# Kernel tuning notes

Hardware: AMD Instinct MI355X
Metric: run time of the kernel (lower is better)

Reference implementation:

```python
import jax, jax.numpy as jnp
import numpy as np

B, V, C = 8192, 512, 16  # batch, num_variables, constraints per variable
N1 = V + 1  # augmented with bias column


def setup_inputs() -> dict:
    key = jax.random.key(0)
    k1, k2, k3 = jax.random.split(key, 3)
    preds = jax.random.normal(k1, (B, V), dtype=jnp.float32)
    # Acyclic structure: variable v's constraints only reference earlier
    # variables (columns < v) plus the bias column (column V).
    cols = jnp.arange(N1)[None, :]              # [1, N1]
    vids = jnp.arange(V)[:, None]               # [V, 1]
    mask = ((cols < vids) | (cols == V)).astype(jnp.float32)[:, None, :]  # [V,1,N1]
    scale = 0.1
    pos_mats = jax.random.normal(k2, (V, C, N1), dtype=jnp.float32) * scale * mask
    neg_mats = jax.random.normal(k3, (V, C, N1), dtype=jnp.float32) * scale * mask
    return {"preds": preds, "pos_mats": pos_mats, "neg_mats": neg_mats}


def reference(preds, pos_mats, neg_mats):
    # Augment preds with a ones column (bias), as in the original __call__.
    b = preds.shape[0]
    p0 = jnp.concatenate([preds, jnp.ones((b, 1), preds.dtype)], axis=1)  # [B, N1]
    var_ids = jnp.arange(pos_mats.shape[0])

    def step(p, xs):
        pm, nm, v = xs  # pm, nm: [C, N1]
        # apply_matrix: (preds * matrix).sum(-1) with max / min reduction over C
        lower = jnp.einsum('bn,cn->bc', p, pm).max(axis=1)  # [B]
        upper = jnp.einsum('bn,cn->bc', p, nm).min(axis=1)  # [B]
        # get_final_x_correction: clamp prediction into [lower, upper]
        corrected = jnp.minimum(jnp.maximum(p[:, v], lower), upper)
        p = p.at[:, v].set(corrected)
        return p, None

    pf, _ = jax.lax.scan(step, p0, (pos_mats, neg_mats, var_ids))
    return pf[:, : preds.shape[1]]
```

## Files before the change

kernel.cpp:

```cpp
#include <hip/hip_runtime.h>

#define BATCH 8192
#define V 512
#define N1 513
#define KCH 16
#define NCHUNKS 32
#define RB 16
#define NT 1024
#define PKS 520
#define SJ2 516

typedef __bf16 bf16_t;
typedef bf16_t bf16x8 __attribute__((ext_vector_type(8)));
typedef float f32x4 __attribute__((ext_vector_type(4)));

#define EPP 4194304ull
#define DV_OFF (EPP * 2ull)
#define BV_OFF (DV_OFF + 1048576ull)

__device__ __forceinline__ f32x4 mfma16(bf16x8 a, bf16x8 b, f32x4 c) {
    return __builtin_amdgcn_mfma_f32_16x16x32_bf16(a, b, c, 0, 0, 0);
}

__device__ __forceinline__ float bcast_lane(float x, int l) {
    return __int_as_float(__builtin_amdgcn_readlane(__float_as_int(x), l));
}

__device__ __forceinline__ float dpp_xor1_max(float x) {
    const int xi = __float_as_int(x);
    const float o = __int_as_float(
        __builtin_amdgcn_update_dpp(xi, xi, 0xB1, 0xF, 0xF, false));
    return fmaxf(x, o);
}

__global__ __launch_bounds__(1024)
void repack_all(const float* __restrict__ pos, const float* __restrict__ neg,
                bf16_t* __restrict__ Mhi, float* __restrict__ Dv,
                float* __restrict__ Bv)
{
    __shared__ float sb[2 * 256 * 36];
    const int bx  = blockIdx.x;
    const int tid = threadIdx.x;
    if (bx < 496) {
        const int cc  = (bx >> 4) + 1;
        const int kb  = bx & 15;
        const int nkb = (cc + 1) >> 1;
        if (kb >= nkb) return;
        const int klen = 16 * cc;
        for (int idx = tid; idx < 8192; idx += 1024) {
            const int r = idx >> 5, k32 = idx & 31;
            const int k = kb * 32 + k32;
            const size_t row = (size_t)cc * 256 + r;
            float xp = 0.0f, xn = 0.0f;
            if (k < klen) {
                xp = pos[row * N1 + k];
                xn = -neg[row * N1 + k];
            }
            sb[r * 36 + k32]            = xp;
            sb[256 * 36 + r * 36 + k32] = xn;
        }
        __syncthreads();
        const size_t base = 16384ull * (size_t)((cc * cc) / 4) + (size_t)kb * 16384ull;
        for (int e8 = tid; e8 < 2048; e8 += 1024) {
            const int t = e8 >> 6, s = e8 & 63;
            const int c = s & 15, q = s >> 4;
            const int vloc = t >> 1, m = t & 1;
            const float* sp = &sb[m * 256 * 36 + (vloc * 16 + c) * 36 + 8 * q];
            bf16x8 o;
            #pragma unroll
            for (int jj = 0; jj < 8; ++jj) o[jj] = (bf16_t)sp[jj];
            *(bf16x8*)(Mhi + base + (size_t)e8 * 8) = o;
        }
    } else {
        const int cc = bx - 496;
        float* bufP = sb;
        float* bufN = sb + 256 * 17;
        for (int idx = tid; idx < 4096; idx += 1024) {
            const int r = idx >> 4, kk = idx & 15;
            const size_t row = (size_t)(cc * 256 + r);
            bufP[r * 17 + kk] = pos[row * N1 + cc * 16 + kk];
            bufN[r * 17 + kk] = neg[row * N1 + cc * 16 + kk];
        }
        __syncthreads();
        for (int idx = tid; idx < 8192; idx += 1024) {
            const int vl = idx >> 9, j = idx & 511;
            const int vlo = j >> 5, c = j & 15;
            const int m = (j >> 4) & 1;
            const float x = (m ? bufN : bufP)[(vlo * 16 + c) * 17 + vl];
            Dv[(size_t)cc * 8192 + idx] = m ? -x : x;
        }
        for (int j = tid; j < 512; j += 1024) {
            const int vlo = j >> 5, c = j & 15;
            const int m = (j >> 4) & 1;
            const float* src = m ? neg : pos;
            const float x = src[(size_t)(cc * 256 + vlo * 16 + c) * N1 + V];
            Bv[(size_t)cc * 512 + j] = m ? -x : x;
        }
    }
}

__global__ __launch_bounds__(NT, 8)
void shield_fused(const float* __restrict__ preds,
                  const bf16_t* __restrict__ Mhi,
                  const float* __restrict__ Dv, const float* __restrict__ Bv,
                  float* __restrict__ out)
{
    __shared__ bf16_t Phi[RB * PKS];
    __shared__ float  S[RB * SJ2];

    const int tid  = threadIdx.x;
    const int b0   = blockIdx.x * RB;
    const int lane = tid & 63;
    const int w    = tid >> 6;
    const int cq   = lane & 15;
    const int q    = lane >> 4;

    {
        const float* prow = preds + (size_t)(b0 + w) * V + lane * 8;
        const float4 p0 = *(const float4*)(prow);
        const float4 p1 = *(const float4*)(prow + 4);
        const int n = lane * 8;
        Phi[w * PKS + n + 0] = (bf16_t)p0.x;
        Phi[w * PKS + n + 1] = (bf16_t)p0.y;
        Phi[w * PKS + n + 2] = (bf16_t)p0.z;
        Phi[w * PKS + n + 3] = (bf16_t)p0.w;
        Phi[w * PKS + n + 4] = (bf16_t)p1.x;
        Phi[w * PKS + n + 5] = (bf16_t)p1.y;
        Phi[w * PKS + n + 6] = (bf16_t)p1.z;
        Phi[w * PKS + n + 7] = (bf16_t)p1.w;
    }

    int tJ[2];
    #pragma unroll
    for (int tt = 0; tt < 2; ++tt) tJ[tt] = ((2 * w + tt) << 4) + cq;
    const int aoff = cq * PKS + 8 * q;

    f32x4 acc[2];
    #pragma unroll
    for (int tt = 0; tt < 2; ++tt) {
        const float b = Bv[tJ[tt]];
        acc[tt] = f32x4{b, b, b, b};
    }

    #pragma unroll 1
    for (int cc = 0; cc < NCHUNKS; ++cc) {
        const int v0 = cc * 16;
        const int  ccn  = cc + 1;
        const bool hasN = ccn < NCHUNKS;
        const int  nkbN = hasN ? ((ccn + 1) >> 1) : 0;
        const bf16_t* phN = Mhi + 16384ull * (size_t)((ccn * ccn) / 4)
                          + (size_t)lane * 8 + (size_t)(2 * w) * 512;

        #pragma unroll
        for (int tt = 0; tt < 2; ++tt)
            #pragma unroll
            for (int reg = 0; reg < 4; ++reg)
                S[(4 * q + reg) * SJ2 + tJ[tt]] = acc[tt][reg];
        __syncthreads();

        float s2[8];
        {
            const float* sp = &S[w * SJ2 + 8 * lane];
            const float4 a0 = *(const float4*)(sp);
            const float4 a1 = *(const float4*)(sp + 4);
            s2[0] = a0.x; s2[1] = a0.y; s2[2] = a0.z; s2[3] = a0.w;
            s2[4] = a1.x; s2[5] = a1.y; s2[6] = a1.z; s2[7] = a1.w;
        }

        const bf16x8 po0 = *(const bf16x8*)(Phi + w * PKS + v0);
        const bf16x8 po1 = *(const bf16x8*)(Phi + w * PKS + v0 + 8);

        if (hasN) {
            #pragma unroll
            for (int tt = 0; tt < 2; ++tt) {
                const float b = Bv[(ccn << 9) + tJ[tt]];
                acc[tt] = f32x4{b, b, b, b};
            }
        }

        __syncthreads();

        {
            const float* src = Dv + (((size_t)cc * 16 + w) << 9) + 8 * lane;
            const float4 a = *(const float4*)(src);
            const float4 b = *(const float4*)(src + 4);
            float* dst = S + w * 512 + 8 * lane;
            *(float4*)(dst)     = a;
            *(float4*)(dst + 4) = b;
        }
        __syncthreads();

        #pragma unroll
        for (int vl = 0; vl < KCH; ++vl) {
            const int vcur = v0 + vl;
            const bool doKb = hasN && (vl < nkbN - 1);

            bf16x8 fa, fb0, fb1;
            if (doKb) {
                const int k0 = vl * 32;
                fa  = *(const bf16x8*)(Phi + aoff + k0);
                const bf16_t* pb = phN + (size_t)k0 * 512;
                fb0 = *(const bf16x8*)(pb);
                fb1 = *(const bf16x8*)(pb + 512);
            }

            float dv[8];
            {
                const float* dls = S + vl * 512 + 8 * lane;
                const float4 d0 = *(const float4*)(dls);
                const float4 d1 = *(const float4*)(dls + 4);
                dv[0]=d0.x; dv[1]=d0.y; dv[2]=d0.z; dv[3]=d0.w;
                dv[4]=d1.x; dv[5]=d1.y; dv[6]=d1.z; dv[7]=d1.w;
            }
            const float po = (float)(vl < 8 ? po0[vl & 7] : po1[vl & 7]);

            const float m0 = fmaxf(fmaxf(s2[0], s2[1]), s2[2]);
            const float m1 = fmaxf(fmaxf(s2[3], s2[4]), s2[5]);
            const float m2 = fmaxf(s2[6], s2[7]);
            const float red = dpp_xor1_max(fmaxf(fmaxf(m0, m1), m2));
            const float lw  = bcast_lane(red, 4 * vl);
            const float nup = bcast_lane(red, 4 * vl + 2);
            const float pc  = fminf(fmaxf(po, lw), -nup);
            if (lane == 4 * vl) Phi[w * PKS + vcur] = (bf16_t)pc;

            #pragma unroll
            for (int jj = 0; jj < 8; ++jj) s2[jj] = fmaf(dv[jj], pc, s2[jj]);

            if (doKb) {
                acc[0] = mfma16(fa, fb0, acc[0]);
                acc[1] = mfma16(fa, fb1, acc[1]);
            }
        }

        __syncthreads();

        if (hasN) {
            const int k0 = (nkbN - 1) * 32;
            const bf16x8 fa  = *(const bf16x8*)(Phi + aoff + k0);
            const bf16_t* pb = phN + (size_t)k0 * 512;
            const bf16x8 fb0 = *(const bf16x8*)(pb);
            const bf16x8 fb1 = *(const bf16x8*)(pb + 512);
            acc[0] = mfma16(fa, fb0, acc[0]);
            acc[1] = mfma16(fa, fb1, acc[1]);
        }
    }

    {
        float* orow = out + (size_t)(b0 + w) * V + lane * 8;
        const int n = lane * 8;
        float4 o0, o1;
        o0.x = (float)Phi[w * PKS + n + 0];
        o0.y = (float)Phi[w * PKS + n + 1];
        o0.z = (float)Phi[w * PKS + n + 2];
        o0.w = (float)Phi[w * PKS + n + 3];
        o1.x = (float)Phi[w * PKS + n + 4];
        o1.y = (float)Phi[w * PKS + n + 5];
        o1.z = (float)Phi[w * PKS + n + 6];
        o1.w = (float)Phi[w * PKS + n + 7];
        *(float4*)(orow)     = o0;
        *(float4*)(orow + 4) = o1;
    }
}

extern "C" void kernel_launch(void* const* d_in, const int* in_sizes, int n_in,
                              void* d_out, int out_size, void* d_ws, size_t ws_size,
                              hipStream_t stream) {
    const float* preds = (const float*)d_in[0];
    const float* pos   = (const float*)d_in[1];
    const float* neg   = (const float*)d_in[2];
    float* o = (float*)d_out;
    char* base = (char*)d_ws;
    bf16_t* Mhi = (bf16_t*)base;
    float*  Dv  = (float*)(base + DV_OFF);
    float*  Bv  = (float*)(base + BV_OFF);
    repack_all<<<dim3(528), 1024, 0, stream>>>(pos, neg, Mhi, Dv, Bv);
    shield_fused<<<dim3(BATCH / RB), NT, 0, stream>>>(preds, Mhi, Dv, Bv, o);
}
```

Measured before the change: 356.5 us.

## Swizzle shared-memory S layout and prefetch Dv chunk before the barrier

Applies an XOR swizzle (lane bit 2) to the float4 addresses used to write and read the S shared buffer, for both the accumulator transpose and the Dv staging. The aim is to cut LDS bank conflicts on the strided 8-float-per-lane accesses. It also issues the global Dv loads at the top of each chunk iteration, so their latency overlaps the S transpose and barriers. The cost is extra address arithmetic and two more float4 registers held live across the barriers.

```diff
diff --git a/kernel.cpp b/kernel.cpp
--- a/kernel.cpp
+++ b/kernel.cpp
@@ -114,6 +114,7 @@
     const int w    = tid >> 6;
     const int cq   = lane & 15;
     const int q    = lane >> 4;
+    const int sw4  = lane & 4;
 
     {
         const float* prow = preds + (size_t)(b0 + w) * V + lane * 8;
@@ -130,9 +131,12 @@
         Phi[w * PKS + n + 7] = (bf16_t)p1.w;
     }
 
-    int tJ[2];
+    int tJ[2], tJs[2];
     #pragma unroll
-    for (int tt = 0; tt < 2; ++tt) tJ[tt] = ((2 * w + tt) << 4) + cq;
+    for (int tt = 0; tt < 2; ++tt) {
+        tJ[tt]  = ((2 * w + tt) << 4) + cq;
+        tJs[tt] = ((2 * w + tt) << 4) + (cq ^ ((w & 1) << 2));
+    }
     const int aoff = cq * PKS + 8 * q;
 
     f32x4 acc[2];
@@ -151,18 +155,25 @@
         const bf16_t* phN = Mhi + 16384ull * (size_t)((ccn * ccn) / 4)
                           + (size_t)lane * 8 + (size_t)(2 * w) * 512;
 
+        float4 dsa, dsb;
+        {
+            const float* src = Dv + (((size_t)cc * 16 + w) << 9) + 8 * lane;
+            dsa = *(const float4*)(src);
+            dsb = *(const float4*)(src + 4);
+        }
+
         #pragma unroll
         for (int tt = 0; tt < 2; ++tt)
             #pragma unroll
             for (int reg = 0; reg < 4; ++reg)
-                S[(4 * q + reg) * SJ2 + tJ[tt]] = acc[tt][reg];
+                S[(4 * q + reg) * SJ2 + tJs[tt]] = acc[tt][reg];
         __syncthreads();
 
         float s2[8];
         {
-            const float* sp = &S[w * SJ2 + 8 * lane];
-            const float4 a0 = *(const float4*)(sp);
-            const float4 a1 = *(const float4*)(sp + 4);
+            const float* sp = &S[w * SJ2];
+            const float4 a0 = *(const float4*)(sp + ((8 * lane) ^ sw4));
+            const float4 a1 = *(const float4*)(sp + ((8 * lane + 4) ^ sw4));
             s2[0] = a0.x; s2[1] = a0.y; s2[2] = a0.z; s2[3] = a0.w;
             s2[4] = a1.x; s2[5] = a1.y; s2[6] = a1.z; s2[7] = a1.w;
         }
@@ -181,12 +192,9 @@
         __syncthreads();
 
         {
-            const float* src = Dv + (((size_t)cc * 16 + w) << 9) + 8 * lane;
-            const float4 a = *(const float4*)(src);
-            const float4 b = *(const float4*)(src + 4);
-            float* dst = S + w * 512 + 8 * lane;
-            *(float4*)(dst)     = a;
-            *(float4*)(dst + 4) = b;
+            float* dst = S + w * 512;
+            *(float4*)(dst + ((8 * lane) ^ sw4))     = dsa;
+            *(float4*)(dst + ((8 * lane + 4) ^ sw4)) = dsb;
         }
         __syncthreads();
 
@@ -206,9 +214,9 @@
 
             float dv[8];
             {
-                const float* dls = S + vl * 512 + 8 * lane;
-                const float4 d0 = *(const float4*)(dls);
-                const float4 d1 = *(const float4*)(dls + 4);
+                const float* dls = S + vl * 512;
+                const float4 d0 = *(const float4*)(dls + ((8 * lane) ^ sw4));
+                const float4 d1 = *(const float4*)(dls + ((8 * lane + 4) ^ sw4));
                 dv[0]=d0.x; dv[1]=d0.y; dv[2]=d0.z; dv[3]=d0.w;
                 dv[4]=d1.x; dv[5]=d1.y; dv[6]=d1.z; dv[7]=d1.w;
             }
```

Result: slower. 366.9 us (+2.9%).

## Process four batch rows per wave with 32-row blocks and prefetched B fragments

Applied to the files above, without the earlier changes.

Doubles the batch rows per block to 32 and halves the threads to 512 (8 waves), so each wave now runs the sequential clamp for four rows at once using f32x4 vector max/fma, and does a 2x4 MFMA tile per k-step instead of 1x2. This reuses each B fragment loaded from global memory across twice as many rows and amortises per-step scalar work. It also software-prefetches the next B fragments and the next Dv row from shared memory. It trades more registers per thread (launch bounds relaxed to 2 blocks) and a larger shared memory footprint for fewer blocks and more instruction-level parallelism, which may lower occupancy.

```diff
diff --git a/kernel.cpp b/kernel.cpp
--- a/kernel.cpp
+++ b/kernel.cpp
@@ -5,8 +5,8 @@
 #define N1 513
 #define KCH 16
 #define NCHUNKS 32
-#define RB 16
-#define NT 1024
+#define RB 32
+#define NT 512
 #define PKS 520
 #define SJ2 516
 
@@ -99,7 +99,7 @@
     }
 }
 
-__global__ __launch_bounds__(NT, 8)
+__global__ __launch_bounds__(NT, 2)
 void shield_fused(const float* __restrict__ preds,
                   const bf16_t* __restrict__ Mhi,
                   const float* __restrict__ Dv, const float* __restrict__ Bv,
@@ -114,32 +114,37 @@
     const int w    = tid >> 6;
     const int cq   = lane & 15;
     const int q    = lane >> 4;
-
-    {
-        const float* prow = preds + (size_t)(b0 + w) * V + lane * 8;
+    const int rp0  = w * 4;
+
+    #pragma unroll
+    for (int i = 0; i < 4; ++i) {
+        const int row = rp0 + i;
+        const float* prow = preds + (size_t)(b0 + row) * V + lane * 8;
         const float4 p0 = *(const float4*)(prow);
         const float4 p1 = *(const float4*)(prow + 4);
         const int n = lane * 8;
-        Phi[w * PKS + n + 0] = (bf16_t)p0.x;
-        Phi[w * PKS + n + 1] = (bf16_t)p0.y;
-        Phi[w * PKS + n + 2] = (bf16_t)p0.z;
-        Phi[w * PKS + n + 3] = (bf16_t)p0.w;
-        Phi[w * PKS + n + 4] = (bf16_t)p1.x;
-        Phi[w * PKS + n + 5] = (bf16_t)p1.y;
-        Phi[w * PKS + n + 6] = (bf16_t)p1.z;
-        Phi[w * PKS + n + 7] = (bf16_t)p1.w;
-    }
-
-    int tJ[2];
+        Phi[row * PKS + n + 0] = (bf16_t)p0.x;
+        Phi[row * PKS + n + 1] = (bf16_t)p0.y;
+        Phi[row * PKS + n + 2] = (bf16_t)p0.z;
+        Phi[row * PKS + n + 3] = (bf16_t)p0.w;
+        Phi[row * PKS + n + 4] = (bf16_t)p1.x;
+        Phi[row * PKS + n + 5] = (bf16_t)p1.y;
+        Phi[row * PKS + n + 6] = (bf16_t)p1.z;
+        Phi[row * PKS + n + 7] = (bf16_t)p1.w;
+    }
+
+    int tJ[4];
     #pragma unroll
-    for (int tt = 0; tt < 2; ++tt) tJ[tt] = ((2 * w + tt) << 4) + cq;
-    const int aoff = cq * PKS + 8 * q;
-
-    f32x4 acc[2];
+    for (int tt = 0; tt < 4; ++tt) tJ[tt] = ((4 * w + tt) << 4) + cq;
+    const int aoff0 = cq * PKS + 8 * q;
+    const int aoff1 = (16 + cq) * PKS + 8 * q;
+
+    f32x4 acc[2][4];
     #pragma unroll
-    for (int tt = 0; tt < 2; ++tt) {
+    for (int tt = 0; tt < 4; ++tt) {
         const float b = Bv[tJ[tt]];
-        acc[tt] = f32x4{b, b, b, b};
+        acc[0][tt] = f32x4{b, b, b, b};
+        acc[1][tt] = f32x4{b, b, b, b};
     }
 
     #pragma unroll 1
@@ -149,86 +154,152 @@
         const bool hasN = ccn < NCHUNKS;
         const int  nkbN = hasN ? ((ccn + 1) >> 1) : 0;
         const bf16_t* phN = Mhi + 16384ull * (size_t)((ccn * ccn) / 4)
-                          + (size_t)lane * 8 + (size_t)(2 * w) * 512;
+                          + (size_t)lane * 8 + (size_t)(4 * w) * 512;
 
         #pragma unroll
-        for (int tt = 0; tt < 2; ++tt)
-            #pragma unroll
-            for (int reg = 0; reg < 4; ++reg)
-                S[(4 * q + reg) * SJ2 + tJ[tt]] = acc[tt][reg];
-        __syncthreads();
-
-        float s2[8];
+        for (int tt = 0; tt < 4; ++tt)
+            #pragma unroll
+            for (int reg = 0; reg < 4; ++reg) {
+                S[(4 * q + reg) * SJ2 + tJ[tt]]      = acc[0][tt][reg];
+                S[(16 + 4 * q + reg) * SJ2 + tJ[tt]] = acc[1][tt][reg];
+            }
+        __syncthreads();
+
+        f32x4 s2[8];
         {
-            const float* sp = &S[w * SJ2 + 8 * lane];
+            const float* sp = &S[rp0 * SJ2 + 8 * lane];
             const float4 a0 = *(const float4*)(sp);
             const float4 a1 = *(const float4*)(sp + 4);
-            s2[0] = a0.x; s2[1] = a0.y; s2[2] = a0.z; s2[3] = a0.w;
-            s2[4] = a1.x; s2[5] = a1.y; s2[6] = a1.z; s2[7] = a1.w;
-        }
-
-        const bf16x8 po0 = *(const bf16x8*)(Phi + w * PKS + v0);
-        const bf16x8 po1 = *(const bf16x8*)(Phi + w * PKS + v0 + 8);
+            const float4 b0_ = *(const float4*)(sp + SJ2);
+            const float4 b1_ = *(const float4*)(sp + SJ2 + 4);
+            const float4 c0 = *(const float4*)(sp + 2 * SJ2);
+            const float4 c1 = *(const float4*)(sp + 2 * SJ2 + 4);
+            const float4 d0 = *(const float4*)(sp + 3 * SJ2);
+            const float4 d1 = *(const float4*)(sp + 3 * SJ2 + 4);
+            s2[0] = f32x4{a0.x, b0_.x, c0.x, d0.x};
+            s2[1] = f32x4{a0.y, b0_.y, c0.y, d0.y};
+            s2[2] = f32x4{a0.z, b0_.z, c0.z, d0.z};
+            s2[3] = f32x4{a0.w, b0_.w, c0.w, d0.w};
+            s2[4] = f32x4{a1.x, b1_.x, c1.x, d1.x};
+            s2[5] = f32x4{a1.y, b1_.y, c1.y, d1.y};
+            s2[6] = f32x4{a1.z, b1_.z, c1.z, d1.z};
+            s2[7] = f32x4{a1.w, b1_.w, c1.w, d1.w};
+        }
+
+        bf16x8 poL[4], poH[4];
+        #pragma unroll
+        for (int r = 0; r < 4; ++r) {
+            poL[r] = *(const bf16x8*)(Phi + (rp0 + r) * PKS + v0);
+            poH[r] = *(const bf16x8*)(Phi + (rp0 + r) * PKS + v0 + 8);
+        }
 
         if (hasN) {
             #pragma unroll
-            for (int tt = 0; tt < 2; ++tt) {
+            for (int tt = 0; tt < 4; ++tt) {
                 const float b = Bv[(ccn << 9) + tJ[tt]];
-                acc[tt] = f32x4{b, b, b, b};
-            }
-        }
-
-        __syncthreads();
-
-        {
-            const float* src = Dv + (((size_t)cc * 16 + w) << 9) + 8 * lane;
+                acc[0][tt] = f32x4{b, b, b, b};
+                acc[1][tt] = f32x4{b, b, b, b};
+            }
+        }
+
+        bf16x8 fbn0, fbn1, fbn2, fbn3;
+        if (hasN) {
+            fbn0 = *(const bf16x8*)(phN);
+            fbn1 = *(const bf16x8*)(phN + 512);
+            fbn2 = *(const bf16x8*)(phN + 1024);
+            fbn3 = *(const bf16x8*)(phN + 1536);
+        }
+
+        __syncthreads();
+
+        #pragma unroll
+        for (int i = 0; i < 2; ++i) {
+            const int vr = 2 * w + i;
+            const float* src = Dv + (((size_t)cc * 16 + vr) << 9) + 8 * lane;
             const float4 a = *(const float4*)(src);
             const float4 b = *(const float4*)(src + 4);
-            float* dst = S + w * 512 + 8 * lane;
+            float* dst = S + vr * 512 + 8 * lane;
             *(float4*)(dst)     = a;
             *(float4*)(dst + 4) = b;
         }
         __syncthreads();
+
+        float dvn[8];
+        {
+            const float* dls = S + 8 * lane;
+            const float4 d0 = *(const float4*)(dls);
+            const float4 d1 = *(const float4*)(dls + 4);
+            dvn[0]=d0.x; dvn[1]=d0.y; dvn[2]=d0.z; dvn[3]=d0.w;
+            dvn[4]=d1.x; dvn[5]=d1.y; dvn[6]=d1.z; dvn[7]=d1.w;
+        }
 
         #pragma unroll
         for (int vl = 0; vl < KCH; ++vl) {
             const int vcur = v0 + vl;
             const bool doKb = hasN && (vl < nkbN - 1);
 
-            bf16x8 fa, fb0, fb1;
+            bf16x8 fb0, fb1, fb2, fb3, fa0, fa1;
             if (doKb) {
+                fb0 = fbn0; fb1 = fbn1; fb2 = fbn2; fb3 = fbn3;
+                const bf16_t* g = phN + (size_t)(vl + 1) * 16384;
+                fbn0 = *(const bf16x8*)(g);
+                fbn1 = *(const bf16x8*)(g + 512);
+                fbn2 = *(const bf16x8*)(g + 1024);
+                fbn3 = *(const bf16x8*)(g + 1536);
                 const int k0 = vl * 32;
-                fa  = *(const bf16x8*)(Phi + aoff + k0);
-                const bf16_t* pb = phN + (size_t)k0 * 512;
-                fb0 = *(const bf16x8*)(pb);
-                fb1 = *(const bf16x8*)(pb + 512);
-            }
-
-            float dv[8];
-            {
-                const float* dls = S + vl * 512 + 8 * lane;
+                fa0 = *(const bf16x8*)(Phi + aoff0 + k0);
+                fa1 = *(const bf16x8*)(Phi + aoff1 + k0);
+            }
+
+            float dvc[8];
+            #pragma unroll
+            for (int jj = 0; jj < 8; ++jj) dvc[jj] = dvn[jj];
+            if (vl + 1 < KCH) {
+                const float* dls = S + (vl + 1) * 512 + 8 * lane;
                 const float4 d0 = *(const float4*)(dls);
                 const float4 d1 = *(const float4*)(dls + 4);
-                dv[0]=d0.x; dv[1]=d0.y; dv[2]=d0.z; dv[3]=d0.w;
-                dv[4]=d1.x; dv[5]=d1.y; dv[6]=d1.z; dv[7]=d1.w;
-            }
-            const float po = (float)(vl < 8 ? po0[vl & 7] : po1[vl & 7]);
-
-            const float m0 = fmaxf(fmaxf(s2[0], s2[1]), s2[2]);
-            const float m1 = fmaxf(fmaxf(s2[3], s2[4]), s2[5]);
-            const float m2 = fmaxf(s2[6], s2[7]);
-            const float red = dpp_xor1_max(fmaxf(fmaxf(m0, m1), m2));
-            const float lw  = bcast_lane(red, 4 * vl);
-            const float nup = bcast_lane(red, 4 * vl + 2);
-            const float pc  = fminf(fmaxf(po, lw), -nup);
-            if (lane == 4 * vl) Phi[w * PKS + vcur] = (bf16_t)pc;
-
-            #pragma unroll
-            for (int jj = 0; jj < 8; ++jj) s2[jj] = fmaf(dv[jj], pc, s2[jj]);
+                dvn[0]=d0.x; dvn[1]=d0.y; dvn[2]=d0.z; dvn[3]=d0.w;
+                dvn[4]=d1.x; dvn[5]=d1.y; dvn[6]=d1.z; dvn[7]=d1.w;
+            }
+
+            const f32x4 m01 = __builtin_elementwise_max(s2[0], s2[1]);
+            const f32x4 m23 = __builtin_elementwise_max(s2[2], s2[3]);
+            const f32x4 m45 = __builtin_elementwise_max(s2[4], s2[5]);
+            const f32x4 m67 = __builtin_elementwise_max(s2[6], s2[7]);
+            const f32x4 mx  = __builtin_elementwise_max(
+                                  __builtin_elementwise_max(m01, m23),
+                                  __builtin_elementwise_max(m45, m67));
+            float pc[4];
+            #pragma unroll
+            for (int r = 0; r < 4; ++r) {
+                const float red = dpp_xor1_max(mx[r]);
+                const float lw  = bcast_lane(red, 4 * vl);
+                const float nup = bcast_lane(red, 4 * vl + 2);
+                const float po  = (float)(vl < 8 ? poL[r][vl & 7]
+                                                 : poH[r][vl & 7]);
+                pc[r] = fminf(fmaxf(po, lw), -nup);
+            }
+            if (lane == 4 * vl) {
+                #pragma unroll
+                for (int r = 0; r < 4; ++r)
+                    Phi[(rp0 + r) * PKS + vcur] = (bf16_t)pc[r];
+            }
+            const f32x4 pcv = {pc[0], pc[1], pc[2], pc[3]};
+            #pragma unroll
+            for (int jj = 0; jj < 8; ++jj) {
+                const f32x4 dsp = {dvc[jj], dvc[jj], dvc[jj], dvc[jj]};
+                s2[jj] = __builtin_elementwise_fma(dsp, pcv, s2[jj]);
+            }
 
             if (doKb) {
-                acc[0] = mfma16(fa, fb0, acc[0]);
-                acc[1] = mfma16(fa, fb1, acc[1]);
+                acc[0][0] = mfma16(fa0, fb0, acc[0][0]);
+                acc[1][0] = mfma16(fa1, fb0, acc[1][0]);
+                acc[0][1] = mfma16(fa0, fb1, acc[0][1]);
+                acc[1][1] = mfma16(fa1, fb1, acc[1][1]);
+                acc[0][2] = mfma16(fa0, fb2, acc[0][2]);
+                acc[1][2] = mfma16(fa1, fb2, acc[1][2]);
+                acc[0][3] = mfma16(fa0, fb3, acc[0][3]);
+                acc[1][3] = mfma16(fa1, fb3, acc[1][3]);
             }
         }
 
@@ -236,27 +307,33 @@
 
         if (hasN) {
             const int k0 = (nkbN - 1) * 32;
-            const bf16x8 fa  = *(const bf16x8*)(Phi + aoff + k0);
-            const bf16_t* pb = phN + (size_t)k0 * 512;
-            const bf16x8 fb0 = *(const bf16x8*)(pb);
-            const bf16x8 fb1 = *(const bf16x8*)(pb + 512);
-            acc[0] = mfma16(fa, fb0, acc[0]);
-            acc[1] = mfma16(fa, fb1, acc[1]);
-        }
-    }
-
-    {
-        float* orow = out + (size_t)(b0 + w) * V + lane * 8;
+            const bf16x8 fa0 = *(const bf16x8*)(Phi + aoff0 + k0);
+            const bf16x8 fa1 = *(const bf16x8*)(Phi + aoff1 + k0);
+            acc[0][0] = mfma16(fa0, fbn0, acc[0][0]);
+            acc[1][0] = mfma16(fa1, fbn0, acc[1][0]);
+            acc[0][1] = mfma16(fa0, fbn1, acc[0][1]);
+            acc[1][1] = mfma16(fa1, fbn1, acc[1][1]);
+            acc[0][2] = mfma16(fa0, fbn2, acc[0][2]);
+            acc[1][2] = mfma16(fa1, fbn2, acc[1][2]);
+            acc[0][3] = mfma16(fa0, fbn3, acc[0][3]);
+            acc[1][3] = mfma16(fa1, fbn3, acc[1][3]);
+        }
+    }
+
+    #pragma unroll
+    for (int i = 0; i < 4; ++i) {
+        const int row = rp0 + i;
+        float* orow = out + (size_t)(b0 + row) * V + lane * 8;
         const int n = lane * 8;
         float4 o0, o1;
-        o0.x = (float)Phi[w * PKS + n + 0];
-        o0.y = (float)Phi[w * PKS + n + 1];
-        o0.z = (float)Phi[w * PKS + n + 2];
-        o0.w = (float)Phi[w * PKS + n + 3];
-        o1.x = (float)Phi[w * PKS + n + 4];
-        o1.y = (float)Phi[w * PKS + n + 5];
-        o1.z = (float)Phi[w * PKS + n + 6];
-        o1.w = (float)Phi[w * PKS + n + 7];
+        o0.x = (float)Phi[row * PKS + n + 0];
+        o0.y = (float)Phi[row * PKS + n + 1];
+        o0.z = (float)Phi[row * PKS + n + 2];
+        o0.w = (float)Phi[row * PKS + n + 3];
+        o1.x = (float)Phi[row * PKS + n + 4];
+        o1.y = (float)Phi[row * PKS + n + 5];
+        o1.z = (float)Phi[row * PKS + n + 6];
+        o1.w = (float)Phi[row * PKS + n + 7];
         *(float4*)(orow)     = o0;
         *(float4*)(orow + 4) = o1;
     }
```

After: 454.3 us. +27.4%, slower.
